# Kernel optimization log

Measured on AMD Instinct MI355X. Metric: run time of the kernel, lower is better.

## Reference

```python
import jax, jax.numpy as jnp
import numpy as np


def setup_inputs() -> dict:
    key = jax.random.key(0)
    k1, k2, k3 = jax.random.split(key, 3)
    B, C_in, H, W = 16, 256, 64, 64
    C_out, KH, KW = 256, 3, 3
    x = jax.random.normal(k1, (B, C_in, H, W), dtype=jnp.float32)
    # kaiming-uniform-like scale for realism
    fan_in = C_in * KH * KW
    bound = 1.0 / np.sqrt(fan_in)
    weights = jax.random.normal(k2, (C_out, C_in, KH, KW), dtype=jnp.float32) * bound
    bias = jax.random.uniform(k3, (C_out,), dtype=jnp.float32, minval=-bound, maxval=bound)
    return {"x": x, "weights": weights, "bias": bias}


def reference(x, weights, bias):
    # Conv2dApproximation with approximation_enable=False is an exact conv2d:
    # input is unfolded to [B, C*kh*kw, oh, ow], weights to [C_out, C*kh*kw],
    # and the MultiApp kernel performs the exact MAC (see exact matmul backward).
    # stride=(1,1), padding=(0,0), dilation=(1,1) per init_kwargs.
    out = jax.lax.conv_general_dilated(
        x, weights,
        window_strides=(1, 1),
        padding=((0, 0), (0, 0)),
        rhs_dilation=(1, 1),
        dimension_numbers=("NCHW", "OIHW", "NCHW"),
    )
    return out + bias[None, :, None, None]
```

## Files before the change

kernel.cpp:

```cpp
#include <hip/hip_runtime.h>
#include <stdint.h>

typedef short short8 __attribute__((ext_vector_type(8)));
typedef float f32x4 __attribute__((ext_vector_type(4)));

#define AS1 __attribute__((address_space(1)))
#define AS3 __attribute__((address_space(3)))

__device__ __forceinline__ void gl_lds16(const void* g, void* l) {
  __builtin_amdgcn_global_load_lds((const AS1 unsigned int*)g,
                                   (AS3 unsigned int*)l, 16, 0, 0);
}

__device__ __forceinline__ unsigned short f2bf(float f) {
  union { float f; unsigned int u; } v; v.f = f;
  return (unsigned short)((v.u + (((v.u >> 16) & 1u) + 0x7fffu)) >> 16);
}

__global__ __launch_bounds__(256) void xpose_kernel(const float* __restrict__ x,
                                                    unsigned short* __restrict__ xt) {
  __shared__ float tile[64][68];
  const int bid = blockIdx.x;
  const int cchunk = bid & 3;
  const int y = (bid >> 2) & 63;
  const int b = bid >> 8;
  const int t = threadIdx.x;
  const int ci0 = cchunk * 64;

  const int cc = t >> 2;
  const int xo = (t & 3) * 16;
  const float* src = x + (((size_t)(b * 256 + ci0 + cc) * 64 + y) * 64 + xo);
  float4 v0 = ((const float4*)src)[0];
  float4 v1 = ((const float4*)src)[1];
  float4 v2 = ((const float4*)src)[2];
  float4 v3 = ((const float4*)src)[3];
  *(float4*)&tile[cc][xo + 0]  = v0;
  *(float4*)&tile[cc][xo + 4]  = v1;
  *(float4*)&tile[cc][xo + 8]  = v2;
  *(float4*)&tile[cc][xo + 12] = v3;
  __syncthreads();

  const int xpos = t >> 2;
  const int ccg = (t & 3) * 16;
  unsigned int pk[8];
#pragma unroll
  for (int e = 0; e < 8; ++e) {
    unsigned int lo = f2bf(tile[ccg + 2 * e][xpos]);
    unsigned int hi = f2bf(tile[ccg + 2 * e + 1][xpos]);
    pk[e] = lo | (hi << 16);
  }
  unsigned short* dst = xt + ((size_t)(b * 4096 + y * 64 + xpos) * 256 + ci0 + ccg);
  uint4 w0; w0.x = pk[0]; w0.y = pk[1]; w0.z = pk[2]; w0.w = pk[3];
  uint4 w1; w1.x = pk[4]; w1.y = pk[5]; w1.z = pk[6]; w1.w = pk[7];
  ((uint4*)dst)[0] = w0;
  ((uint4*)dst)[1] = w1;
}

__global__ __launch_bounds__(256) void wpack_kernel(const float* __restrict__ w,
                                                    unsigned short* __restrict__ wrp) {
  const int idx = blockIdx.x * 256 + threadIdx.x;
  const int ci = idx & 255;
  const int co = (idx >> 8) & 255;
  const int p = idx >> 16;
  wrp[idx] = f2bf(w[(size_t)(co * 256 + ci) * 9 + p]);
}

__global__ __launch_bounds__(512, 2) void conv_8ph(
    const unsigned short* __restrict__ xt,
    const unsigned short* __restrict__ wrp,
    const float* __restrict__ bias,
    float* __restrict__ out) {
  __shared__ unsigned short lds[2][32768];

  const int tid = threadIdx.x;
  const int lane = tid & 63;
  const int wv = tid >> 6;
  const int wm = wv >> 2;
  const int wn = wv & 3;
  const int bid = blockIdx.x;
  const int tile = (bid & 7) * 32 + (bid >> 3);
  const int b = tile >> 4;
  const int oh0 = (tile & 15) * 4;

  const int crow = tid >> 3;
  const int cslot = tid & 7;
  const int sw = cslot ^ (crow & 7);
  const unsigned short* gAbase = wrp + (size_t)crow * 256 + sw * 8;
  const unsigned short* gBbase[4];
#pragma unroll
  for (int cb = 0; cb < 4; ++cb) {
    const int y = min(oh0 + cb, 61);
    const int x = min(crow, 61);
    gBbase[cb] = xt + ((size_t)(b * 64 + y) * 64 + x) * 256 + sw * 8;
  }
  const unsigned dst_rc = crow * 64 + cslot * 8;

  const int l15 = lane & 15;
  int s8[2];
  s8[0] = (((lane >> 4)) ^ (lane & 7)) * 8;
  s8[1] = (((lane >> 4) + 4) ^ (lane & 7)) * 8;
  int arow[8], brow[4];
#pragma unroll
  for (int a = 0; a < 8; ++a)
    arow[a] = (wm * 128 + (a >> 2) * 64 + (a & 3) * 16 + l15) * 64;
#pragma unroll
  for (int n = 0; n < 4; ++n)
    brow[n] = 16384 + (wn * 64 + n * 16 + l15) * 64;

  auto stageA = [&](int kt2, int c, unsigned short* bufp) {
    const int tap = kt2 >> 2, ci0 = (kt2 & 3) * 64;
    gl_lds16(gAbase + tap * 65536 + c * 16384 + ci0, bufp + c * 4096 + dst_rc);
  };
  auto stageB = [&](int kt2, int cb, unsigned short* bufp) {
    const int tap = kt2 >> 2, ci0 = (kt2 & 3) * 64;
    const int kh = (tap * 11) >> 5, kw = tap - kh * 3;
    gl_lds16(gBbase[cb] + (kh * 64 + kw) * 256 + ci0, bufp + (4 + cb) * 4096 + dst_rc);
  };

  f32x4 acc[8][4] = {};
  unsigned short* buf0 = &lds[0][0];
  unsigned short* buf1 = &lds[1][0];

  stageA(0, 0, buf0); stageA(0, 2, buf0); stageA(0, 1, buf0); stageA(0, 3, buf0);
  stageB(0, 2, buf0); stageB(0, 3, buf0); stageB(0, 0, buf0); stageB(0, 1, buf0);
  stageB(1, 0, buf1); stageB(1, 1, buf1);
  asm volatile("s_waitcnt vmcnt(2)" ::: "memory");
  __builtin_amdgcn_s_barrier();

  for (int kt = 0; kt < 36; ++kt) {
    unsigned short* buf = (kt & 1) ? buf1 : buf0;
    unsigned short* nbuf = (kt & 1) ? buf0 : buf1;
    short8 a0[4], a1[4], bb[4];

#pragma unroll
    for (int q = 0; q < 4; ++q) a0[q] = *(const short8*)(buf + arow[q] + s8[0]);
#pragma unroll
    for (int n = 0; n < 4; ++n) bb[n] = *(const short8*)(buf + brow[n] + s8[0]);
    if (kt < 35) { stageA(kt + 1, 0, nbuf); stageA(kt + 1, 2, nbuf); }
    __builtin_amdgcn_s_barrier();
    asm volatile("s_waitcnt lgkmcnt(0)" ::: "memory");
    __builtin_amdgcn_sched_barrier(0);
    __builtin_amdgcn_s_setprio(1);
#pragma unroll
    for (int q = 0; q < 4; ++q)
#pragma unroll
      for (int n = 0; n < 4; ++n)
        acc[q][n] = __builtin_amdgcn_mfma_f32_16x16x32_bf16(a0[q], bb[n], acc[q][n], 0, 0, 0);
    __builtin_amdgcn_s_setprio(0);
    __builtin_amdgcn_s_barrier();

#pragma unroll
    for (int q = 0; q < 4; ++q) a1[q] = *(const short8*)(buf + arow[4 + q] + s8[0]);
    if (kt < 35) { stageA(kt + 1, 1, nbuf); stageA(kt + 1, 3, nbuf); }
    __builtin_amdgcn_s_barrier();
    asm volatile("s_waitcnt lgkmcnt(0)" ::: "memory");
    __builtin_amdgcn_sched_barrier(0);
    __builtin_amdgcn_s_setprio(1);
#pragma unroll
    for (int q = 0; q < 4; ++q)
#pragma unroll
      for (int n = 0; n < 4; ++n)
        acc[4 + q][n] = __builtin_amdgcn_mfma_f32_16x16x32_bf16(a1[q], bb[n], acc[4 + q][n], 0, 0, 0);
    __builtin_amdgcn_s_setprio(0);
    __builtin_amdgcn_s_barrier();

#pragma unroll
    for (int q = 0; q < 4; ++q) a0[q] = *(const short8*)(buf + arow[q] + s8[1]);
#pragma unroll
    for (int n = 0; n < 4; ++n) bb[n] = *(const short8*)(buf + brow[n] + s8[1]);
    if (kt < 35) { stageB(kt + 1, 2, nbuf); stageB(kt + 1, 3, nbuf); }
    __builtin_amdgcn_s_barrier();
    asm volatile("s_waitcnt lgkmcnt(0)" ::: "memory");
    __builtin_amdgcn_sched_barrier(0);
    __builtin_amdgcn_s_setprio(1);
#pragma unroll
    for (int q = 0; q < 4; ++q)
#pragma unroll
      for (int n = 0; n < 4; ++n)
        acc[q][n] = __builtin_amdgcn_mfma_f32_16x16x32_bf16(a0[q], bb[n], acc[q][n], 0, 0, 0);
    __builtin_amdgcn_s_setprio(0);
    __builtin_amdgcn_s_barrier();

#pragma unroll
    for (int q = 0; q < 4; ++q) a1[q] = *(const short8*)(buf + arow[4 + q] + s8[1]);
    if (kt < 34) { stageB(kt + 2, 0, buf); stageB(kt + 2, 1, buf); }
    __builtin_amdgcn_s_barrier();
    asm volatile("s_waitcnt lgkmcnt(0)" ::: "memory");
    __builtin_amdgcn_sched_barrier(0);
    __builtin_amdgcn_s_setprio(1);
#pragma unroll
    for (int q = 0; q < 4; ++q)
#pragma unroll
      for (int n = 0; n < 4; ++n)
        acc[4 + q][n] = __builtin_amdgcn_mfma_f32_16x16x32_bf16(a1[q], bb[n], acc[4 + q][n], 0, 0, 0);
    __builtin_amdgcn_s_setprio(0);
    if (kt < 34)       asm volatile("s_waitcnt vmcnt(2)" ::: "memory");
    else if (kt == 34) asm volatile("s_waitcnt vmcnt(0)" ::: "memory");
    __builtin_amdgcn_s_barrier();
  }

  const int rb = (lane >> 4) * 4;
  const int colp = lane & 15;
#pragma unroll
  for (int a = 0; a < 8; ++a) {
    const int co = wm * 128 + (a >> 2) * 64 + (a & 3) * 16 + rb;
    float bv[4];
#pragma unroll
    for (int j = 0; j < 4; ++j) bv[j] = bias[co + j];
#pragma unroll
    for (int n = 0; n < 4; ++n) {
      const int px = wn * 64 + n * 16 + colp;
      const int prow = px >> 6, ow = px & 63;
      const int oh = oh0 + prow;
      if (ow < 62 && oh < 62) {
#pragma unroll
        for (int j = 0; j < 4; ++j)
          out[((size_t)(b * 256 + co + j) * 62 + oh) * 62 + ow] = acc[a][n][j] + bv[j];
      }
    }
  }
}

__global__ __launch_bounds__(256) void conv_naive(const float* __restrict__ x,
                                                  const float* __restrict__ wgt,
                                                  const float* __restrict__ bias,
                                                  float* __restrict__ out) {
  const size_t idx = (size_t)blockIdx.x * 256 + threadIdx.x;
  if (idx >= (size_t)16 * 256 * 62 * 62) return;
  const int ow = (int)(idx % 62);
  size_t r = idx / 62;
  const int oh = (int)(r % 62); r /= 62;
  const int co = (int)(r % 256);
  const int b = (int)(r / 256);
  float s = bias[co];
  for (int ci = 0; ci < 256; ++ci) {
    const float* xp = x + ((size_t)(b * 256 + ci) * 64 + oh) * 64 + ow;
    const float* wp = wgt + (size_t)(co * 256 + ci) * 9;
#pragma unroll
    for (int kh = 0; kh < 3; ++kh)
#pragma unroll
      for (int kw = 0; kw < 3; ++kw)
        s += xp[kh * 64 + kw] * wp[kh * 3 + kw];
  }
  out[idx] = s;
}

extern "C" void kernel_launch(void* const* d_in, const int* in_sizes, int n_in,
                              void* d_out, int out_size, void* d_ws, size_t ws_size,
                              hipStream_t stream) {
  const float* x = (const float*)d_in[0];
  const float* wgt = (const float*)d_in[1];
  const float* bias = (const float*)d_in[2];
  float* out = (float*)d_out;

  const size_t xt_elems = (size_t)16 * 64 * 64 * 256;
  const size_t wr_elems = (size_t)9 * 256 * 256;
  const size_t need = (xt_elems + wr_elems) * sizeof(unsigned short);

  if (ws_size < need) {
    conv_naive<<<61504, 256, 0, stream>>>(x, wgt, bias, out);
    return;
  }

  unsigned short* xt = (unsigned short*)d_ws;
  unsigned short* wrp = xt + xt_elems;

  xpose_kernel<<<4096, 256, 0, stream>>>(x, xt);
  wpack_kernel<<<2304, 256, 0, stream>>>(wgt, wrp);
  conv_8ph<<<256, 512, 0, stream>>>(xt, wrp, bias, out);
}
```

Baseline: 97.53 us.

## Restructure conv main loop with register-prefetched fragments and one barrier per k-step

Replaces the four-barrier-per-iteration schedule with a software pipeline. Each k-step's A and B tiles are fully staged into the other LDS buffer, and MFMA fragments are double-buffered in registers so LDS reads for the next phase overlap the current MFMAs. Only one barrier per k-tile remains, right after a full vmcnt/lgkmcnt wait. This cuts barrier and sync overhead, but drops the earlier two-step-ahead B prefetch, so global-load latency may be exposed at the single wait point, and register pressure rises.

Measured after the change: 89.07 us. 8.7% less time.

```diff
diff --git a/kernel.cpp b/kernel.cpp
--- a/kernel.cpp
+++ b/kernel.cpp
@@ -65,7 +65,7 @@
   wrp[idx] = f2bf(w[(size_t)(co * 256 + ci) * 9 + p]);
 }
 
-__global__ __launch_bounds__(512, 2) void conv_8ph(
+__global__ __launch_bounds__(512, 2) void conv_pipe(
     const unsigned short* __restrict__ xt,
     const unsigned short* __restrict__ wrp,
     const float* __restrict__ bias,
@@ -96,9 +96,9 @@
   const unsigned dst_rc = crow * 64 + cslot * 8;
 
   const int l15 = lane & 15;
-  int s8[2];
-  s8[0] = (((lane >> 4)) ^ (lane & 7)) * 8;
-  s8[1] = (((lane >> 4) + 4) ^ (lane & 7)) * 8;
+  int s8v[2];
+  s8v[0] = (((lane >> 4)) ^ (lane & 7)) * 8;
+  s8v[1] = (((lane >> 4) + 4) ^ (lane & 7)) * 8;
   int arow[8], brow[4];
 #pragma unroll
   for (int a = 0; a < 8; ++a)
@@ -107,96 +107,95 @@
   for (int n = 0; n < 4; ++n)
     brow[n] = 16384 + (wn * 64 + n * 16 + l15) * 64;
 
-  auto stageA = [&](int kt2, int c, unsigned short* bufp) {
+  auto stageA = [&](int kt2, unsigned short* bufp) {
     const int tap = kt2 >> 2, ci0 = (kt2 & 3) * 64;
-    gl_lds16(gAbase + tap * 65536 + c * 16384 + ci0, bufp + c * 4096 + dst_rc);
+    const unsigned short* g = gAbase + tap * 65536 + ci0;
+#pragma unroll
+    for (int c = 0; c < 4; ++c)
+      gl_lds16(g + c * 16384, bufp + c * 4096 + dst_rc);
   };
-  auto stageB = [&](int kt2, int cb, unsigned short* bufp) {
+  auto stageB = [&](int kt2, unsigned short* bufp) {
     const int tap = kt2 >> 2, ci0 = (kt2 & 3) * 64;
     const int kh = (tap * 11) >> 5, kw = tap - kh * 3;
-    gl_lds16(gBbase[cb] + (kh * 64 + kw) * 256 + ci0, bufp + (4 + cb) * 4096 + dst_rc);
+    const int off = (kh * 64 + kw) * 256 + ci0;
+#pragma unroll
+    for (int cb = 0; cb < 4; ++cb)
+      gl_lds16(gBbase[cb] + off, bufp + (4 + cb) * 4096 + dst_rc);
   };
 
   f32x4 acc[8][4] = {};
   unsigned short* buf0 = &lds[0][0];
   unsigned short* buf1 = &lds[1][0];
 
-  stageA(0, 0, buf0); stageA(0, 2, buf0); stageA(0, 1, buf0); stageA(0, 3, buf0);
-  stageB(0, 2, buf0); stageB(0, 3, buf0); stageB(0, 0, buf0); stageB(0, 1, buf0);
-  stageB(1, 0, buf1); stageB(1, 1, buf1);
-  asm volatile("s_waitcnt vmcnt(2)" ::: "memory");
+  stageA(0, buf0);
+  stageB(0, buf0);
+  asm volatile("s_waitcnt vmcnt(0)" ::: "memory");
   __builtin_amdgcn_s_barrier();
 
+  short8 a_cur[4], b_cur[4], a_nxt[4], b_nxt[4];
+#pragma unroll
+  for (int q = 0; q < 4; ++q) a_cur[q] = *(const short8*)(buf0 + arow[q] + s8v[0]);
+#pragma unroll
+  for (int n = 0; n < 4; ++n) b_cur[n] = *(const short8*)(buf0 + brow[n] + s8v[0]);
+
   for (int kt = 0; kt < 36; ++kt) {
-    unsigned short* buf = (kt & 1) ? buf1 : buf0;
+    const unsigned short* buf = (kt & 1) ? buf1 : buf0;
     unsigned short* nbuf = (kt & 1) ? buf0 : buf1;
-    short8 a0[4], a1[4], bb[4];
-
-#pragma unroll
-    for (int q = 0; q < 4; ++q) a0[q] = *(const short8*)(buf + arow[q] + s8[0]);
-#pragma unroll
-    for (int n = 0; n < 4; ++n) bb[n] = *(const short8*)(buf + brow[n] + s8[0]);
-    if (kt < 35) { stageA(kt + 1, 0, nbuf); stageA(kt + 1, 2, nbuf); }
-    __builtin_amdgcn_s_barrier();
-    asm volatile("s_waitcnt lgkmcnt(0)" ::: "memory");
-    __builtin_amdgcn_sched_barrier(0);
-    __builtin_amdgcn_s_setprio(1);
-#pragma unroll
-    for (int q = 0; q < 4; ++q)
-#pragma unroll
-      for (int n = 0; n < 4; ++n)
-        acc[q][n] = __builtin_amdgcn_mfma_f32_16x16x32_bf16(a0[q], bb[n], acc[q][n], 0, 0, 0);
-    __builtin_amdgcn_s_setprio(0);
-    __builtin_amdgcn_s_barrier();
-
-#pragma unroll
-    for (int q = 0; q < 4; ++q) a1[q] = *(const short8*)(buf + arow[4 + q] + s8[0]);
-    if (kt < 35) { stageA(kt + 1, 1, nbuf); stageA(kt + 1, 3, nbuf); }
-    __builtin_amdgcn_s_barrier();
-    asm volatile("s_waitcnt lgkmcnt(0)" ::: "memory");
-    __builtin_amdgcn_sched_barrier(0);
-    __builtin_amdgcn_s_setprio(1);
-#pragma unroll
-    for (int q = 0; q < 4; ++q)
-#pragma unroll
-      for (int n = 0; n < 4; ++n)
-        acc[4 + q][n] = __builtin_amdgcn_mfma_f32_16x16x32_bf16(a1[q], bb[n], acc[4 + q][n], 0, 0, 0);
-    __builtin_amdgcn_s_setprio(0);
-    __builtin_amdgcn_s_barrier();
-
-#pragma unroll
-    for (int q = 0; q < 4; ++q) a0[q] = *(const short8*)(buf + arow[q] + s8[1]);
-#pragma unroll
-    for (int n = 0; n < 4; ++n) bb[n] = *(const short8*)(buf + brow[n] + s8[1]);
-    if (kt < 35) { stageB(kt + 1, 2, nbuf); stageB(kt + 1, 3, nbuf); }
-    __builtin_amdgcn_s_barrier();
-    asm volatile("s_waitcnt lgkmcnt(0)" ::: "memory");
-    __builtin_amdgcn_sched_barrier(0);
-    __builtin_amdgcn_s_setprio(1);
-#pragma unroll
-    for (int q = 0; q < 4; ++q)
-#pragma unroll
-      for (int n = 0; n < 4; ++n)
-        acc[q][n] = __builtin_amdgcn_mfma_f32_16x16x32_bf16(a0[q], bb[n], acc[q][n], 0, 0, 0);
-    __builtin_amdgcn_s_setprio(0);
-    __builtin_amdgcn_s_barrier();
-
-#pragma unroll
-    for (int q = 0; q < 4; ++q) a1[q] = *(const short8*)(buf + arow[4 + q] + s8[1]);
-    if (kt < 34) { stageB(kt + 2, 0, buf); stageB(kt + 2, 1, buf); }
-    __builtin_amdgcn_s_barrier();
-    asm volatile("s_waitcnt lgkmcnt(0)" ::: "memory");
-    __builtin_amdgcn_sched_barrier(0);
-    __builtin_amdgcn_s_setprio(1);
-#pragma unroll
-    for (int q = 0; q < 4; ++q)
-#pragma unroll
-      for (int n = 0; n < 4; ++n)
-        acc[4 + q][n] = __builtin_amdgcn_mfma_f32_16x16x32_bf16(a1[q], bb[n], acc[4 + q][n], 0, 0, 0);
-    __builtin_amdgcn_s_setprio(0);
-    if (kt < 34)       asm volatile("s_waitcnt vmcnt(2)" ::: "memory");
-    else if (kt == 34) asm volatile("s_waitcnt vmcnt(0)" ::: "memory");
-    __builtin_amdgcn_s_barrier();
+
+#pragma unroll
+    for (int q = 0; q < 4; ++q) a_nxt[q] = *(const short8*)(buf + arow[4 + q] + s8v[0]);
+    if (kt < 35) stageA(kt + 1, nbuf);
+    __builtin_amdgcn_sched_barrier(0);
+    __builtin_amdgcn_s_setprio(1);
+#pragma unroll
+    for (int q = 0; q < 4; ++q)
+#pragma unroll
+      for (int n = 0; n < 4; ++n)
+        acc[q][n] = __builtin_amdgcn_mfma_f32_16x16x32_bf16(a_cur[q], b_cur[n], acc[q][n], 0, 0, 0);
+    __builtin_amdgcn_s_setprio(0);
+
+#pragma unroll
+    for (int q = 0; q < 4; ++q) a_cur[q] = *(const short8*)(buf + arow[q] + s8v[1]);
+#pragma unroll
+    for (int n = 0; n < 4; ++n) b_nxt[n] = *(const short8*)(buf + brow[n] + s8v[1]);
+    if (kt < 35) stageB(kt + 1, nbuf);
+    __builtin_amdgcn_sched_barrier(0);
+    __builtin_amdgcn_s_setprio(1);
+#pragma unroll
+    for (int q = 0; q < 4; ++q)
+#pragma unroll
+      for (int n = 0; n < 4; ++n)
+        acc[4 + q][n] = __builtin_amdgcn_mfma_f32_16x16x32_bf16(a_nxt[q], b_cur[n], acc[4 + q][n], 0, 0, 0);
+    __builtin_amdgcn_s_setprio(0);
+
+#pragma unroll
+    for (int q = 0; q < 4; ++q) a_nxt[q] = *(const short8*)(buf + arow[4 + q] + s8v[1]);
+    __builtin_amdgcn_sched_barrier(0);
+    __builtin_amdgcn_s_setprio(1);
+#pragma unroll
+    for (int q = 0; q < 4; ++q)
+#pragma unroll
+      for (int n = 0; n < 4; ++n)
+        acc[q][n] = __builtin_amdgcn_mfma_f32_16x16x32_bf16(a_cur[q], b_nxt[n], acc[q][n], 0, 0, 0);
+    __builtin_amdgcn_s_setprio(0);
+
+    if (kt < 35) {
+      asm volatile("s_waitcnt vmcnt(0)" ::: "memory");
+      asm volatile("s_waitcnt lgkmcnt(0)" ::: "memory");
+      __builtin_amdgcn_s_barrier();
+#pragma unroll
+      for (int q = 0; q < 4; ++q) a_cur[q] = *(const short8*)(nbuf + arow[q] + s8v[0]);
+#pragma unroll
+      for (int n = 0; n < 4; ++n) b_cur[n] = *(const short8*)(nbuf + brow[n] + s8v[0]);
+    }
+    __builtin_amdgcn_sched_barrier(0);
+    __builtin_amdgcn_s_setprio(1);
+#pragma unroll
+    for (int q = 0; q < 4; ++q)
+#pragma unroll
+      for (int n = 0; n < 4; ++n)
+        acc[4 + q][n] = __builtin_amdgcn_mfma_f32_16x16x32_bf16(a_nxt[q], b_nxt[n], acc[4 + q][n], 0, 0, 0);
+    __builtin_amdgcn_s_setprio(0);
   }
 
   const int rb = (lane >> 4) * 4;
@@ -267,5 +266,5 @@
 
   xpose_kernel<<<4096, 256, 0, stream>>>(x, xt);
   wpack_kernel<<<2304, 256, 0, stream>>>(wgt, wrp);
-  conv_8ph<<<256, 512, 0, stream>>>(xt, wrp, bias, out);
-}
+  conv_pipe<<<256, 512, 0, stream>>>(xt, wrp, bias, out);
+}
```
